# Performance work log

Measured on AMD Instinct MI355X. Metric: run time of the kernel, lower is better.

## Reference

```python
import jax, jax.numpy as jnp
import numpy as np

_A1 = jnp.array([[1.,0.,0.,0.],[0.,1.,0.,0.],[0.,0.,1.,0.],[0.,0.,0.,1.]], dtype=jnp.float32)
_AI = jnp.array([[0.,-1.,0.,0.],[1.,0.,0.,0.],[0.,0.,0.,-1.],[0.,0.,1.,0.]], dtype=jnp.float32)
_AJ = jnp.array([[0.,0.,-1.,0.],[0.,0.,0.,1.],[1.,0.,0.,0.],[0.,-1.,0.,0.]], dtype=jnp.float32)
_AK = jnp.array([[0.,0.,0.,-1.],[0.,0.,-1.,0.],[0.,1.,0.,0.],[1.,0.,0.,0.]], dtype=jnp.float32)

IN_FEATURES = 1024
OUT_FEATURES = 1024
Q_IN = IN_FEATURES // 4
Q_OUT = OUT_FEATURES // 4

def _xavier_uniform(key, shape, gain=0.5):
    fan_out, fan_in = shape
    limit = gain * float(np.sqrt(6.0 / (fan_in + fan_out)))
    return jax.random.uniform(key, shape, jnp.float32, -limit, limit)

def setup_inputs() -> dict:
    key = jax.random.key(0)
    kx, kr, ki, kj, kk = jax.random.split(key, 5)
    x = jax.random.normal(kx, (8, 4096, IN_FEATURES), dtype=jnp.float32)
    R = _xavier_uniform(kr, (Q_OUT, Q_IN))
    I = _xavier_uniform(ki, (Q_OUT, Q_IN))
    J = _xavier_uniform(kj, (Q_OUT, Q_IN))
    K = _xavier_uniform(kk, (Q_OUT, Q_IN))
    bias = jnp.zeros((OUT_FEATURES,), dtype=jnp.float32)
    return {"x": x, "R": R, "I": I, "J": J, "K": K, "bias": bias}

def _build_weight(R, I, J, K):
    # W = kron(A1,R) + kron(AI,I) + kron(AJ,J) + kron(AK,K), shape (4*q_out, 4*q_in)
    # Assemble as 4x4 signed block grid in one einsum-style broadcast.
    # blocks[a,b] = A1[a,b]*R + AI[a,b]*I + AJ[a,b]*J + AK[a,b]*K
    blocks = (_A1[:, :, None, None] * R + _AI[:, :, None, None] * I
              + _AJ[:, :, None, None] * J + _AK[:, :, None, None] * K)  # [4,4,qo,qi]
    qo, qi = R.shape
    return blocks.transpose(0, 2, 1, 3).reshape(4 * qo, 4 * qi)

def reference(x, R, I, J, K, bias):
    W = _build_weight(R, I, J, K)
    return jnp.einsum('bsi,oi->bso', x, W) + bias
```

## Files before the change

### kernel.cpp

```cpp
#include <hip/hip_runtime.h>
#include <hip/hip_bf16.h>

typedef __attribute__((ext_vector_type(4))) float f32x4;
typedef __attribute__((ext_vector_type(4))) uint u32x4;
typedef __attribute__((ext_vector_type(8))) short bf16x8;

#define M_TOTAL 32768
#define N_TOTAL 1024
#define K_TOTAL 1024

__device__ __forceinline__ uint pk2(float a, float b) {
  __hip_bfloat162 h = __float22bfloat162_rn(make_float2(a, b));
  uint u;
  __builtin_memcpy(&u, &h, 4);
  return u;
}

#define SOFT_BARRIER() do {                                                   \
    __builtin_amdgcn_sched_barrier(0);                                        \
    asm volatile("s_waitcnt lgkmcnt(0)" ::: "memory");                        \
    __builtin_amdgcn_s_barrier();                                             \
    __builtin_amdgcn_sched_barrier(0);                                        \
  } while (0)

__global__ __launch_bounds__(256) void conv_b(
    const float* __restrict__ Rm, const float* __restrict__ Im,
    const float* __restrict__ Jm, const float* __restrict__ Km,
    ushort* __restrict__ ws)
{
  const int slot = blockIdx.x * 256 + threadIdx.x;
  const int lane = slot & 63;
  const int kb = (slot >> 6) & 7;
  const int cb = (slot >> 9) & 15;
  const int si = slot >> 13;
  const float* S = (si == 0) ? Rm : (si == 1) ? Im : (si == 2) ? Jm : Km;
  const float* p = S + (cb * 16 + (lane & 15)) * 256 + kb * 32 + (lane >> 4) * 8;
  f32x4 lo = *(const f32x4*)p;
  f32x4 hi = *(const f32x4*)(p + 4);
  u32x4 v;
  v[0] = pk2(lo[0], lo[1]); v[1] = pk2(lo[2], lo[3]);
  v[2] = pk2(hi[0], hi[1]); v[3] = pk2(hi[2], hi[3]);
  *(u32x4*)(ws + (size_t)slot * 8) = v;
}

#define BM2 256
#define BN2 256
#define BK2 64
#define NT2 512
#define NSTEPS2 (K_TOTAL / BK2)

#define LOAD_A2(kk) do {                                                      \
    _Pragma("unroll")                                                         \
    for (int cc = 0; cc < 4; ++cc) {                                          \
      const float* pa_ = X + (size_t)(m0 + r0 + 64 * cc) * K_TOTAL + (kk) + k0;\
      rA[2 * cc]     = *(const f32x4*)pa_;                                    \
      rA[2 * cc + 1] = *(const f32x4*)(pa_ + 4);                              \
    }                                                                         \
  } while (0)

#define COMMIT_A2(dst) do {                                                   \
    _Pragma("unroll")                                                         \
    for (int cc = 0; cc < 4; ++cc) {                                          \
      u32x4 va_;                                                              \
      va_[0] = pk2(rA[2 * cc][0], rA[2 * cc][1]);                             \
      va_[1] = pk2(rA[2 * cc][2], rA[2 * cc][3]);                             \
      va_[2] = pk2(rA[2 * cc + 1][0], rA[2 * cc + 1][1]);                     \
      va_[3] = pk2(rA[2 * cc + 1][2], rA[2 * cc + 1][3]);                     \
      *(u32x4*)((dst) + sbase + 8192 * cc) = va_;                             \
    }                                                                         \
  } while (0)

#define LOAD_B2(kk) do {                                                      \
    const int bsel_ = (kk) >> 8;                                              \
    const int si_ = a_idx ^ bsel_;                                            \
    const int kbq_ = ((kk) & 255) >> 5;                                       \
    const ushort* fb_ = WS + ((size_t)((si_ * 16 + wc4) * 8 + kbq_)) * 512    \
                        + lane * 8;                                           \
    _Pragma("unroll")                                                         \
    for (int ks = 0; ks < 2; ++ks)                                            \
      _Pragma("unroll")                                                       \
      for (int ni = 0; ni < 4; ++ni)                                          \
        bq[ks * 4 + ni] = *(const bf16x8*)(fb_ + (ni * 8 + ks) * 512);        \
    if ((0x284Eu >> ((a_idx << 2) | bsel_)) & 1u) {                           \
      _Pragma("unroll")                                                       \
      for (int f = 0; f < 8; ++f) {                                           \
        u32x4 u_ = __builtin_bit_cast(u32x4, bq[f]);                          \
        u_[0] ^= 0x80008000u; u_[1] ^= 0x80008000u;                           \
        u_[2] ^= 0x80008000u; u_[3] ^= 0x80008000u;                           \
        bq[f] = __builtin_bit_cast(bf16x8, u_);                               \
      }                                                                       \
    }                                                                         \
  } while (0)

#define COMPUTE2(src) do {                                                    \
    _Pragma("unroll")                                                         \
    for (int ks = 0; ks < 2; ++ks) {                                          \
      _Pragma("unroll")                                                       \
      for (int mi = 0; mi < 8; ++mi) {                                        \
        const int row_ = frow_a0 + (mi << 4);                                 \
        const int kb_ = (ks << 6) + fkb;                                      \
        bf16x8 af_ = *(const bf16x8*)((src) + row_ * (BK2 * 2)                \
                                      + (kb_ ^ ((row_ & 7) << 4)));           \
        _Pragma("unroll")                                                     \
        for (int ni = 0; ni < 4; ++ni)                                        \
          acc[mi][ni] = __builtin_amdgcn_mfma_f32_16x16x32_bf16(              \
              af_, bq[ks * 4 + ni], acc[mi][ni], 0, 0, 0);                    \
      }                                                                       \
    }                                                                         \
  } while (0)

__global__ __launch_bounds__(NT2, 2) void qlin_gemm2(
    const float* __restrict__ X, const ushort* __restrict__ WS,
    const float* __restrict__ bias, float* __restrict__ Y)
{
  const int per = ((M_TOTAL / BM2) * (N_TOTAL / BN2)) >> 3;
  const int bid = (int)blockIdx.x;
  const int swz = (bid & 7) * per + (bid >> 3);
  const int m0 = (swz >> 2) * BM2;
  const int nblk = swz & 3;
  const int n0 = nblk * BN2;
  const int a_idx = nblk;

  const int tid = (int)threadIdx.x;
  const int lane = tid & 63;
  const int wave = tid >> 6;
  const int wm = (wave >> 2) << 7;
  const int wc4 = (wave & 3) << 2;

  __shared__ __align__(16) ushort smA[2 * BM2 * BK2];
  char* const cS = (char*)smA;

  const int r0 = tid >> 3;
  const int k0 = (tid & 7) << 3;
  const int sbase = r0 * (BK2 * 2) + ((k0 * 2) ^ ((r0 & 7) << 4));

  f32x4 rA[8];
  bf16x8 bq[8];
  f32x4 acc[8][4];
#pragma unroll
  for (int i = 0; i < 8; ++i)
#pragma unroll
    for (int j = 0; j < 4; ++j) acc[i][j] = (f32x4)(0.0f);

  const int frow_a0 = wm + (lane & 15);
  const int fkb = (lane >> 4) << 4;

  LOAD_A2(0);
  COMMIT_A2(cS);
  LOAD_A2(BK2);
  SOFT_BARRIER();

#pragma unroll 1
  for (int k = 0; k < NSTEPS2; ++k) {
    char* const rbuf = cS + ((k & 1) << 15);
    char* const wbuf = cS + (((k + 1) & 1) << 15);
    if (k + 1 < NSTEPS2) { LOAD_A2((k + 1) * BK2); }
    (void)0;
    if (k + 1 < NSTEPS2) { }
    COMMIT_A2(wbuf);
    LOAD_B2(k * BK2);
    if (k + 2 < NSTEPS2) LOAD_A2((k + 2) * BK2);
    COMPUTE2(rbuf);
    SOFT_BARRIER();
  }

#pragma unroll
  for (int ni = 0; ni < 4; ++ni) {
    const int col = n0 + (wc4 << 4) + (ni << 4) + (lane & 15);
    const float bv = bias[col];
#pragma unroll
    for (int mi = 0; mi < 8; ++mi) {
      const int r0e = m0 + wm + (mi << 4) + ((lane >> 4) << 2);
#pragma unroll
      for (int j = 0; j < 4; ++j)
        Y[(size_t)(r0e + j) * N_TOTAL + col] = acc[mi][ni][j] + bv;
    }
  }
}

#define BM 128
#define BN 128
#define BK 64
#define NTHREADS 256
#define NSTEPS (K_TOTAL / BK)

#define LOAD_TILE(kk) do {                                                    \
    const int si_ = a_idx ^ ((kk) >> 8);                                      \
    const float* Bsrc_ = (si_ == 0) ? Rm : (si_ == 1) ? Im                    \
                       : (si_ == 2) ? Jm : Km;                                \
    const int kloc_ = (kk) & 255;                                             \
    _Pragma("unroll")                                                         \
    for (int cc = 0; cc < 4; ++cc) {                                          \
      const float* pa_ = X + (size_t)(m0 + r0 + 32 * cc) * K_TOTAL + (kk) + k0;\
      rA[2 * cc]     = *(const f32x4*)pa_;                                    \
      rA[2 * cc + 1] = *(const f32x4*)(pa_ + 4);                              \
      const float* pb_ = Bsrc_ + (o_src + r0 + 32 * cc) * 256 + kloc_ + k0;   \
      rB[2 * cc]     = *(const f32x4*)pb_;                                    \
      rB[2 * cc + 1] = *(const f32x4*)(pb_ + 4);                              \
    }                                                                         \
  } while (0)

#define COMMIT_TILE(kk, dst) do {                                             \
    const uint neg_ = (0x284Eu >> ((a_idx << 2) | ((kk) >> 8))) & 1u;         \
    _Pragma("unroll")                                                         \
    for (int cc = 0; cc < 4; ++cc) {                                          \
      u32x4 va_;                                                              \
      va_[0] = pk2(rA[2 * cc][0], rA[2 * cc][1]);                             \
      va_[1] = pk2(rA[2 * cc][2], rA[2 * cc][3]);                             \
      va_[2] = pk2(rA[2 * cc + 1][0], rA[2 * cc + 1][1]);                     \
      va_[3] = pk2(rA[2 * cc + 1][2], rA[2 * cc + 1][3]);                     \
      *(u32x4*)((dst) + sbase + 4096 * cc) = va_;                             \
    }                                                                         \
    if (neg_) {                                                               \
      _Pragma("unroll")                                                       \
      for (int cc = 0; cc < 4; ++cc) {                                        \
        u32x4 vb_;                                                            \
        vb_[0] = pk2(-rB[2 * cc][0], -rB[2 * cc][1]);                         \
        vb_[1] = pk2(-rB[2 * cc][2], -rB[2 * cc][3]);                         \
        vb_[2] = pk2(-rB[2 * cc + 1][0], -rB[2 * cc + 1][1]);                 \
        vb_[3] = pk2(-rB[2 * cc + 1][2], -rB[2 * cc + 1][3]);                 \
        *(u32x4*)((dst) + 16384 + sbase + 4096 * cc) = vb_;                   \
      }                                                                       \
    } else {                                                                  \
      _Pragma("unroll")                                                       \
      for (int cc = 0; cc < 4; ++cc) {                                        \
        u32x4 vb_;                                                            \
        vb_[0] = pk2(rB[2 * cc][0], rB[2 * cc][1]);                           \
        vb_[1] = pk2(rB[2 * cc][2], rB[2 * cc][3]);                           \
        vb_[2] = pk2(rB[2 * cc + 1][0], rB[2 * cc + 1][1]);                   \
        vb_[3] = pk2(rB[2 * cc + 1][2], rB[2 * cc + 1][3]);                   \
        *(u32x4*)((dst) + 16384 + sbase + 4096 * cc) = vb_;                   \
      }                                                                       \
    }                                                                         \
  } while (0)

#define COMPUTE_TILE(src) do {                                                \
    _Pragma("unroll")                                                         \
    for (int ks = 0; ks < 2; ++ks) {                                          \
      const int kb_ = (ks << 6) + fkb;                                        \
      bf16x8 af_[4], bf_[4];                                                  \
      _Pragma("unroll")                                                       \
      for (int mi = 0; mi < 4; ++mi) {                                        \
        const int row_ = frow_a0 + (mi << 4);                                 \
        af_[mi] = *(const bf16x8*)((src) + row_ * (BK * 2)                    \
                                   + (kb_ ^ ((row_ & 7) << 4)));              \
      }                                                                       \
      _Pragma("unroll")                                                       \
      for (int ni = 0; ni < 4; ++ni) {                                        \
        const int row_ = frow_b0 + (ni << 4);                                 \
        bf_[ni] = *(const bf16x8*)((src) + 16384 + row_ * (BK * 2)            \
                                   + (kb_ ^ ((row_ & 7) << 4)));              \
      }                                                                       \
      _Pragma("unroll")                                                       \
      for (int mi = 0; mi < 4; ++mi)                                          \
        _Pragma("unroll")                                                     \
        for (int ni = 0; ni < 4; ++ni)                                        \
          acc[mi][ni] = __builtin_amdgcn_mfma_f32_16x16x32_bf16(              \
              af_[mi], bf_[ni], acc[mi][ni], 0, 0, 0);                        \
    }                                                                         \
  } while (0)

__global__ __launch_bounds__(NTHREADS, 2) void qlin_gemm(
    const float* __restrict__ X, const float* __restrict__ Rm,
    const float* __restrict__ Im, const float* __restrict__ Jm,
    const float* __restrict__ Km, const float* __restrict__ bias,
    float* __restrict__ Y)
{
  const int per = ((M_TOTAL / BM) * (N_TOTAL / BN)) >> 3;
  const int bid = (int)blockIdx.x;
  const int swz = (bid & 7) * per + (bid >> 3);
  const int m0 = (swz >> 3) * BM;
  const int n0 = (swz & 7) * BN;

  const int tid = (int)threadIdx.x;
  const int lane = tid & 63;
  const int wave = tid >> 6;
  const int wm = (wave >> 1) << 6;
  const int wn = (wave & 1) << 6;

  __shared__ __align__(16) ushort sm[2 * 2 * BM * BK];
  char* const cS = (char*)sm;

  const int a_idx = n0 >> 8;
  const int o_src = n0 & 255;

  const int r0 = tid >> 3;
  const int k0 = (tid & 7) << 3;
  const int sbase = r0 * (BK * 2) + ((k0 * 2) ^ ((r0 & 7) << 4));

  f32x4 rA[8], rB[8];
  f32x4 acc[4][4];
#pragma unroll
  for (int i = 0; i < 4; ++i)
#pragma unroll
    for (int j = 0; j < 4; ++j) acc[i][j] = (f32x4)(0.0f);

  const int frow_a0 = wm + (lane & 15);
  const int frow_b0 = wn + (lane & 15);
  const int fkb = (lane >> 4) << 4;

  LOAD_TILE(0);
  COMMIT_TILE(0, cS);
  LOAD_TILE(BK);
  SOFT_BARRIER();

#pragma unroll 1
  for (int k = 0; k < NSTEPS; ++k) {
    char* const rbuf = cS + ((k & 1) << 15);
    char* const wbuf = cS + (((k + 1) & 1) << 15);
    if (k + 1 < NSTEPS) COMMIT_TILE((k + 1) * BK, wbuf);
    if (k + 2 < NSTEPS) LOAD_TILE((k + 2) * BK);
    COMPUTE_TILE(rbuf);
    SOFT_BARRIER();
  }

#pragma unroll
  for (int ni = 0; ni < 4; ++ni) {
    const int col = n0 + wn + (ni << 4) + (lane & 15);
    const float bv = bias[col];
#pragma unroll
    for (int mi = 0; mi < 4; ++mi) {
      const int r0e = m0 + wm + (mi << 4) + ((lane >> 4) << 2);
#pragma unroll
      for (int j = 0; j < 4; ++j)
        Y[(size_t)(r0e + j) * N_TOTAL + col] = acc[mi][ni][j] + bv;
    }
  }
}

extern "C" void kernel_launch(void* const* d_in, const int* in_sizes, int n_in,
                              void* d_out, int out_size, void* d_ws, size_t ws_size,
                              hipStream_t stream) {
  const float* X = (const float*)d_in[0];
  const float* Rm = (const float*)d_in[1];
  const float* Im = (const float*)d_in[2];
  const float* Jm = (const float*)d_in[3];
  const float* Km = (const float*)d_in[4];
  const float* bias = (const float*)d_in[5];
  float* Y = (float*)d_out;

  if (ws_size >= (size_t)(4 * 256 * 256 * 2)) {
    ushort* ws = (ushort*)d_ws;
    conv_b<<<dim3(128), dim3(256), 0, stream>>>(Rm, Im, Jm, Km, ws);
    dim3 grid((M_TOTAL / BM2) * (N_TOTAL / BN2));
    qlin_gemm2<<<grid, dim3(NT2), 0, stream>>>(X, ws, bias, Y);
  } else {
    dim3 grid((M_TOTAL / BM) * (N_TOTAL / BN));
    qlin_gemm<<<grid, dim3(NTHREADS), 0, stream>>>(X, Rm, Im, Jm, Km, bias, Y);
  }
}
```

Measured before the change: 116.6 us.

## Pre-pack X to bf16 MFMA-fragment layout and use LDS-free register GEMM

Adds a conversion kernel that writes X as bf16 in a layout matching the MFMA fragments. A new GEMM then loads A and B fragments straight from global memory into registers, double-buffered, with no shared memory or barriers. The weight is built from only the four quaternion blocks: sign flips are applied with XOR on the bf16 sign bits, and the block is chosen per k-quarter. It also drops a redundant A reload in the older GEMM loop. The cost is an extra pass over X and a 64MB workspace requirement. The path is only taken if the workspace is large enough.

```diff
diff --git a/kernel.cpp b/kernel.cpp
--- a/kernel.cpp
+++ b/kernel.cpp
@@ -23,12 +23,30 @@
     __builtin_amdgcn_sched_barrier(0);                                        \
   } while (0)
 
+__global__ __launch_bounds__(256) void conv_x(
+    const float* __restrict__ X, ushort* __restrict__ wsx)
+{
+  const int g = blockIdx.x * 256 + (int)threadIdx.x;
+  const int wid = g >> 6;
+  const int lane = g & 63;
+  const int fm = wid >> 5;
+  const int kb = wid & 31;
+  const float* p = X + (size_t)(fm * 16 + (lane & 15)) * K_TOTAL
+                     + kb * 32 + (lane >> 4) * 8;
+  f32x4 lo = *(const f32x4*)p;
+  f32x4 hi = *(const f32x4*)(p + 4);
+  u32x4 v;
+  v[0] = pk2(lo[0], lo[1]); v[1] = pk2(lo[2], lo[3]);
+  v[2] = pk2(hi[0], hi[1]); v[3] = pk2(hi[2], hi[3]);
+  *(u32x4*)(wsx + (size_t)wid * 512 + lane * 8) = v;
+}
+
 __global__ __launch_bounds__(256) void conv_b(
     const float* __restrict__ Rm, const float* __restrict__ Im,
     const float* __restrict__ Jm, const float* __restrict__ Km,
     ushort* __restrict__ ws)
 {
-  const int slot = blockIdx.x * 256 + threadIdx.x;
+  const int slot = blockIdx.x * 256 + (int)threadIdx.x;
   const int lane = slot & 63;
   const int kb = (slot >> 6) & 7;
   const int cb = (slot >> 9) & 15;
@@ -43,6 +61,99 @@
   *(u32x4*)(ws + (size_t)slot * 8) = v;
 }
 
+#define LOADF(kk, AF, BF) do {                                                \
+    const int kbf0_ = (kk) >> 5;                                              \
+    _Pragma("unroll")                                                         \
+    for (int mi = 0; mi < 4; ++mi)                                            \
+      _Pragma("unroll")                                                       \
+      for (int ks = 0; ks < 2; ++ks)                                          \
+        AF[mi * 2 + ks] = *(const bf16x8*)(                                   \
+            WSX + (size_t)((fm0 + mi) * 32 + kbf0_ + ks) * 512 + lane * 8);   \
+    const int si_ = a_idx ^ ((kk) >> 8);                                      \
+    const int kbq_ = ((kk) & 255) >> 5;                                       \
+    _Pragma("unroll")                                                         \
+    for (int ks = 0; ks < 2; ++ks)                                            \
+      _Pragma("unroll")                                                       \
+      for (int ni = 0; ni < 4; ++ni)                                          \
+        BF[ks * 4 + ni] = *(const bf16x8*)(                                   \
+            WSB + (size_t)((si_ * 16 + cb0 + ni) * 8 + kbq_ + ks) * 512       \
+            + lane * 8);                                                      \
+  } while (0)
+
+#define SGNFIX(kk, BF) do {                                                   \
+    if ((0x284Eu >> ((a_idx << 2) | ((kk) >> 8))) & 1u) {                     \
+      _Pragma("unroll")                                                       \
+      for (int f = 0; f < 8; ++f) {                                           \
+        u32x4 u_ = __builtin_bit_cast(u32x4, BF[f]);                          \
+        u_[0] ^= 0x80008000u; u_[1] ^= 0x80008000u;                           \
+        u_[2] ^= 0x80008000u; u_[3] ^= 0x80008000u;                           \
+        BF[f] = __builtin_bit_cast(bf16x8, u_);                               \
+      }                                                                       \
+    }                                                                         \
+  } while (0)
+
+#define MFMAS(AF, BF) do {                                                    \
+    _Pragma("unroll")                                                         \
+    for (int ks = 0; ks < 2; ++ks)                                            \
+      _Pragma("unroll")                                                       \
+      for (int mi = 0; mi < 4; ++mi)                                          \
+        _Pragma("unroll")                                                     \
+        for (int ni = 0; ni < 4; ++ni)                                        \
+          acc[mi][ni] = __builtin_amdgcn_mfma_f32_16x16x32_bf16(              \
+              AF[mi * 2 + ks], BF[ks * 4 + ni], acc[mi][ni], 0, 0, 0);        \
+  } while (0)
+
+__global__ __launch_bounds__(256, 2) void qlin_gemm5(
+    const ushort* __restrict__ WSX, const ushort* __restrict__ WSB,
+    const float* __restrict__ bias, float* __restrict__ Y)
+{
+  const int per = 2048 >> 3;
+  const int bid = (int)blockIdx.x;
+  const int swz = (bid & 7) * per + (bid >> 3);
+  const int mblk = swz >> 2;
+  const int a_idx = swz & 3;
+  const int n0 = a_idx << 8;
+  const int m0 = mblk << 6;
+  const int fm0 = mblk << 2;
+
+  const int tid = (int)threadIdx.x;
+  const int lane = tid & 63;
+  const int w = tid >> 6;
+  const int cb0 = w << 2;
+
+  bf16x8 A0[8], B0[8], A1[8], B1[8];
+  f32x4 acc[4][4];
+#pragma unroll
+  for (int i = 0; i < 4; ++i)
+#pragma unroll
+    for (int j = 0; j < 4; ++j) acc[i][j] = (f32x4)(0.0f);
+
+  LOADF(0, A0, B0);
+#pragma unroll 1
+  for (int k = 0; k < 16; k += 2) {
+    const int kk0 = k << 6;
+    if (k + 1 < 16) LOADF(kk0 + 64, A1, B1);
+    SGNFIX(kk0, B0);
+    MFMAS(A0, B0);
+    if (k + 2 < 16) LOADF(kk0 + 128, A0, B0);
+    SGNFIX(kk0 + 64, B1);
+    MFMAS(A1, B1);
+  }
+
+#pragma unroll
+  for (int ni = 0; ni < 4; ++ni) {
+    const int col = n0 + (w << 6) + (ni << 4) + (lane & 15);
+    const float bv = bias[col];
+#pragma unroll
+    for (int mi = 0; mi < 4; ++mi) {
+      const int r0e = m0 + (mi << 4) + ((lane >> 4) << 2);
+#pragma unroll
+      for (int j = 0; j < 4; ++j)
+        Y[(size_t)(r0e + j) * N_TOTAL + col] = acc[mi][ni][j] + bv;
+    }
+  }
+}
+
 #define BM2 256
 #define BN2 256
 #define BK2 64
@@ -154,9 +265,6 @@
   for (int k = 0; k < NSTEPS2; ++k) {
     char* const rbuf = cS + ((k & 1) << 15);
     char* const wbuf = cS + (((k + 1) & 1) << 15);
-    if (k + 1 < NSTEPS2) { LOAD_A2((k + 1) * BK2); }
-    (void)0;
-    if (k + 1 < NSTEPS2) { }
     COMMIT_A2(wbuf);
     LOAD_B2(k * BK2);
     if (k + 2 < NSTEPS2) LOAD_A2((k + 2) * BK2);
@@ -339,13 +447,22 @@
   const float* bias = (const float*)d_in[5];
   float* Y = (float*)d_out;
 
-  if (ws_size >= (size_t)(4 * 256 * 256 * 2)) {
-    ushort* ws = (ushort*)d_ws;
-    conv_b<<<dim3(128), dim3(256), 0, stream>>>(Rm, Im, Jm, Km, ws);
-    dim3 grid((M_TOTAL / BM2) * (N_TOTAL / BN2));
-    qlin_gemm2<<<grid, dim3(NT2), 0, stream>>>(X, ws, bias, Y);
+  const size_t needB = (size_t)4 * 256 * 256 * 2;
+  const size_t needX = (size_t)M_TOTAL * K_TOTAL * 2;
+
+  if (ws_size >= needX + needB) {
+    ushort* wsx = (ushort*)d_ws;
+    ushort* wsb = wsx + (size_t)M_TOTAL * K_TOTAL;
+    conv_x<<<dim3(16384), dim3(256), 0, stream>>>(X, wsx);
+    conv_b<<<dim3(128), dim3(256), 0, stream>>>(Rm, Im, Jm, Km, wsb);
+    qlin_gemm5<<<dim3(2048), dim3(256), 0, stream>>>(wsx, wsb, bias, Y);
+  } else if (ws_size >= needB) {
+    ushort* wsb = (ushort*)d_ws;
+    conv_b<<<dim3(128), dim3(256), 0, stream>>>(Rm, Im, Jm, Km, wsb);
+    qlin_gemm2<<<dim3((M_TOTAL / BM2) * (N_TOTAL / BN2)), dim3(NT2), 0, stream>>>(
+        X, wsb, bias, Y);
   } else {
-    dim3 grid((M_TOTAL / BM) * (N_TOTAL / BN));
-    qlin_gemm<<<grid, dim3(NTHREADS), 0, stream>>>(X, Rm, Im, Jm, Km, bias, Y);
-  }
-}
+    qlin_gemm<<<dim3((M_TOTAL / BM) * (N_TOTAL / BN)), dim3(NTHREADS), 0, stream>>>(
+        X, Rm, Im, Jm, Km, bias, Y);
+  }
+}
```

Result: slower. 131.6 us (+12.9%).
